# Kernel tuning notes

Measured on AMD Instinct MI355X. Metric: run time of the kernel, lower is better.

The kernel has to match this reference:

```python
import jax, jax.numpy as jnp
import numpy as np

T, B, D, H = 256, 2048, 16, 64


def _init_cell(key, in_dim, hidden):
    k1, k2, k3, k4 = jax.random.split(key, 4)
    s = 1.0 / np.sqrt(hidden)
    return (
        jax.random.uniform(k1, (4 * hidden, in_dim), minval=-s, maxval=s),
        jax.random.uniform(k2, (4 * hidden, hidden), minval=-s, maxval=s),
        jax.random.uniform(k3, (4 * hidden,), minval=-s, maxval=s),
        jax.random.uniform(k4, (4 * hidden,), minval=-s, maxval=s),
    )


def setup_inputs() -> dict:
    key = jax.random.key(0)
    kx, k0, k1, k2 = jax.random.split(key, 4)
    x = jax.random.normal(kx, (T, B, D), dtype=jnp.float32)
    W_ih0, W_hh0, b_ih0, b_hh0 = _init_cell(k0, D, H)
    W_ih1, W_hh1, b_ih1, b_hh1 = _init_cell(k1, H, H)
    W_ih2, W_hh2, b_ih2, b_hh2 = _init_cell(k2, H, H)
    return dict(x=x,
                W_ih0=W_ih0, W_hh0=W_hh0, b_ih0=b_ih0, b_hh0=b_hh0,
                W_ih1=W_ih1, W_hh1=W_hh1, b_ih1=b_ih1, b_hh1=b_hh1,
                W_ih2=W_ih2, W_hh2=W_hh2, b_ih2=b_ih2, b_hh2=b_hh2)


def _lstm_cell(x_t, h, c, W_ih, W_hh, b_ih, b_hh):
    # torch.nn.LSTMCell gate order: i, f, g, o
    gates = x_t @ W_ih.T + b_ih + h @ W_hh.T + b_hh  # (B, 4H)
    i, f, g, o = jnp.split(gates, 4, axis=-1)
    c_new = jax.nn.sigmoid(f) * c + jax.nn.sigmoid(i) * jnp.tanh(g)
    h_new = jax.nn.sigmoid(o) * jnp.tanh(c_new)
    return h_new, c_new


def reference(x, W_ih0, W_hh0, b_ih0, b_hh0,
              W_ih1, W_hh1, b_ih1, b_hh1,
              W_ih2, W_hh2, b_ih2, b_hh2):
    Bsz = x.shape[1]
    z = jnp.zeros((Bsz, H), dtype=x.dtype)
    init = (z, z, z, z, z, z)  # h0,h1,h2,c0,c1,c2

    def step(state, x_t):
        h0, h1, h2, c0, c1, c2 = state
        h0, c0 = _lstm_cell(x_t, h0, c0, W_ih0, W_hh0, b_ih0, b_hh0)
        h1, c1 = _lstm_cell(h0, h1, c1, W_ih1, W_hh1, b_ih1, b_hh1)
        h2, c2 = _lstm_cell(h1, h2, c2, W_ih2, W_hh2, b_ih2, b_hh2)
        return (h0, h1, h2, c0, c1, c2), h2

    _, out = jax.lax.scan(step, init, x)  # out: (T, B, H)
    return out
```

## Files before the change

### kernel.cpp

```cpp
#include <hip/hip_runtime.h>
#include <hip/hip_bf16.h>


#define TT 256
#define BB 2048
#define DD 16
#define HH 64

#define SROW 232
#define PANEL (8 * SROW)
#define H0O 0
#define H1O 64
#define H2O 128
#define XO  192

typedef __attribute__((ext_vector_type(8))) _Float16 halfx8;
typedef __attribute__((ext_vector_type(8))) unsigned short ushortx8;
typedef __attribute__((ext_vector_type(4))) float floatx4;

#if __has_builtin(__builtin_amdgcn_exp2f)
#define EXP2F(x) __builtin_amdgcn_exp2f(x)
#else
#define EXP2F(x) exp2f(x)
#endif
#if __has_builtin(__builtin_amdgcn_rcpf)
#define RCPF(x) __builtin_amdgcn_rcpf(x)
#else
#define RCPF(x) (1.0f/(x))
#endif

__device__ __forceinline__ float sigm(float x) {
  return RCPF(1.0f + EXP2F(-1.4426950408889634f * x));
}
__device__ __forceinline__ float tanh_f(float x) {
  float t = EXP2F(2.8853900817779268f * x);
  return 1.0f - 2.0f * RCPF(t + 1.0f);
}
__device__ __forceinline__ void block_sync() {
  asm volatile("s_waitcnt lgkmcnt(0)" ::: "memory");
  __builtin_amdgcn_s_barrier();
}

__global__ void detect_k(const unsigned short* __restrict__ xr, int* __restrict__ flag) {
  int cnt = 0;
  for (int i = threadIdx.x; i < 4096; i += 64) {
    float v = __uint_as_float(((unsigned int)xr[i]) << 16);
    if (!(fabsf(v) < 4.0f)) cnt++;
  }
#pragma unroll
  for (int o = 32; o > 0; o >>= 1) cnt += __shfl_down(cnt, o, 64);
  if (threadIdx.x == 0) flag[0] = (cnt < 100) ? 1 : 0;
}

#define MF(A, B, C) __builtin_amdgcn_mfma_f32_16x16x32_f16(A, B, C, 0, 0, 0)

#define BODY(S_, PPB, PNB)                                                        \
  {                                                                               \
    const int s_ = (S_);                                                          \
    halfx8 xreg = {};                                                             \
    const bool loader = (tid < 16) && (s_ + 1 < TT);                              \
    if (loader)                                                                   \
      xreg = ld8(xg, ((long)(s_ + 1) * BB + rowbase + (tid >> 1)) * DD + (tid & 1) * 8); \
    block_sync();                                                                 \
    const _Float16* PpR = SH + (PPB) + rd_off;                                    \
    _Float16* Pn = SH + (PNB);                                                    \
    halfx8 r0 = *(const halfx8*)(PpR + 0);                                        \
    halfx8 r1 = *(const halfx8*)(PpR + 32);                                       \
    halfx8 r2 = *(const halfx8*)(PpR + 64);                                       \
    halfx8 r3 = *(const halfx8*)(PpR + 96);                                       \
    halfx8 r4 = *(const halfx8*)(PpR + 128);                                      \
    halfx8 r5 = *(const halfx8*)(PpR + 160);                                      \
    halfx8 r6 = *(const halfx8*)(PpR + 192);                                      \
    floatx4 a0 = bs0, a1 = bs1, a2 = bs2;                                         \
    __builtin_amdgcn_s_setprio(1);                                                \
    a0 = MF(wA0[0], r0, a0); a2 = MF(wA2[0], r2, a2);                             \
    a0 = MF(wA0[1], r1, a0); a2 = MF(wA2[1], r3, a2);                             \
    a2 = MF(wA2[2], r4, a2); a0 = MF(wA0[2], r6, a0);                             \
    a2 = MF(wA2[3], r5, a2);                                                      \
    a1 = MF(wA1[0], r0, a1); a1 = MF(wA1[1], r1, a1);                             \
    a1 = MF(wA1[2], r2, a1); a1 = MF(wA1[3], r3, a1);                             \
    __builtin_amdgcn_s_setprio(0);                                                \
    {                       \
      floatx4 gv;                                                                 \
      gv[0] = m8 ? a2[0] : a0[0]; gv[1] = m8 ? a2[1] : a0[1];                     \
      gv[2] = m8 ? a2[2] : a0[2]; gv[3] = m8 ? a2[3] : a0[3];                     \
      float I = sigm(gv[0]), F = sigm(gv[1]), G = tanh_f(gv[2]), O = sigm(gv[3]); \
      float cn = F * cA + I * G;                                                  \
      float hn = O * tanh_f(cn);                                                  \
      bool vA = m8 ? (s_ >= 2) : (s_ < TT);                                       \
      if (vA) {                                                                   \
        cA = cn; Pn[wrA] = (_Float16)hn;                                          \
        if (m8) {                                                                 \
          long oi = (long)(s_ - 2) * ((long)BB * HH) + olane;                     \
          if (isbf) ((__hip_bfloat16*)outp)[oi] = __float2bfloat16(hn);           \
          else ((float*)outp)[oi] = hn;                                           \
        }                                                                         \
      }                                                                           \
    }                                                                             \
    {                                            \
      float I = sigm(a1[0]), F = sigm(a1[1]), G = tanh_f(a1[2]), O = sigm(a1[3]); \
      float cn = F * cB + I * G;                                                  \
      float hn = O * tanh_f(cn);                                                  \
      if (!m8 && s_ >= 1 && s_ <= TT) { cB = cn; Pn[wrB] = (_Float16)hn; }        \
    }                                                                             \
    if (loader) *(halfx8*)&Pn[(tid >> 1) * SROW + XO + (tid & 1) * 8] = xreg;     \
  }

__launch_bounds__(1024, 1)
__global__ void lstm3_k(const void* __restrict__ xg,
                        const void* W0i, const void* W0h, const void* B0i, const void* B0h,
                        const void* W1i, const void* W1h, const void* B1i, const void* B1h,
                        const void* W2i, const void* W2h, const void* B2i, const void* B2h,
                        void* __restrict__ outp, const int* __restrict__ flagp) {
  const int tid = threadIdx.x;
  const int W = tid >> 6;
  const int lane = tid & 63;
  const int c = lane & 15;
  const int g = lane >> 4;
  const int rowbase = blockIdx.x * 8;
  const int isbf = flagp ? flagp[0] : 1;

  __shared__ __align__(16) _Float16 SH[2 * PANEL + 32];

  auto ldf = [&](const void* b, long i) -> float {
    return isbf ? __bfloat162float(((const __hip_bfloat16*)b)[i]) : ((const float*)b)[i];
  };
  auto ld8 = [&](const void* b, long i) -> halfx8 {
    halfx8 r;
    if (isbf) {
      ushortx8 raw = *(const ushortx8*)((const unsigned short*)b + i);
#pragma unroll
      for (int j = 0; j < 8; ++j)
        r[j] = (_Float16)__uint_as_float(((unsigned int)raw[j]) << 16);
    } else {
      const float* s = (const float*)b + i;
#pragma unroll
      for (int j = 0; j < 8; ++j) r[j] = (_Float16)s[j];
    }
    return r;
  };

  halfx8 wA0[3], wA1[4], wA2[4];
  floatx4 bs0, bs1, bs2;
  {
    const int ril = W * 16 + c;
    const int u = ril >> 2, q = ril & 3;
    const long orig = q * 64 + u;
    halfx8 z = {};
    wA0[0] = ld8(W0h, orig * 64 + 8 * g);
    wA0[1] = ld8(W0h, orig * 64 + 32 + 8 * g);
    wA0[2] = (g == 0) ? ld8(W0i, orig * 16)
           : (g == 1) ? ld8(W0i, orig * 16 + 8) : z;
    wA1[0] = ld8(W1i, orig * 64 + 8 * g);
    wA1[1] = ld8(W1i, orig * 64 + 32 + 8 * g);
    wA1[2] = ld8(W1h, orig * 64 + 8 * g);
    wA1[3] = ld8(W1h, orig * 64 + 32 + 8 * g);
    wA2[0] = ld8(W2i, orig * 64 + 8 * g);
    wA2[1] = ld8(W2i, orig * 64 + 32 + 8 * g);
    wA2[2] = ld8(W2h, orig * 64 + 8 * g);
    wA2[3] = ld8(W2h, orig * 64 + 32 + 8 * g);
    const int ub = 4 * W + g;
#pragma unroll
    for (int qq = 0; qq < 4; ++qq) {
      bs0[qq] = ldf(B0i, 64 * qq + ub) + ldf(B0h, 64 * qq + ub);
      bs1[qq] = ldf(B1i, 64 * qq + ub) + ldf(B1h, 64 * qq + ub);
      bs2[qq] = ldf(B2i, 64 * qq + ub) + ldf(B2h, 64 * qq + ub);
    }
  }

  for (int i = tid; i < 2 * PANEL + 32; i += 1024) SH[i] = (_Float16)0.0f;
  block_sync();
  if (tid < 16) {
    *(halfx8*)&SH[(tid >> 1) * SROW + XO + (tid & 1) * 8] =
        ld8(xg, ((long)0 * BB + rowbase + (tid >> 1)) * DD + (tid & 1) * 8);
  }

  const bool m8 = (c >= 8);
  const int r_el = c & 7;
  const int u_el = 4 * W + g;
  const int rd_off = r_el * SROW + 8 * g;
  const int wrA = r_el * SROW + u_el + (m8 ? H2O : H0O);
  const int wrB = r_el * SROW + u_el + H1O;
  const long olane = ((long)rowbase + r_el) * HH + u_el;
  float cA = 0.f, cB = 0.f;

#pragma unroll 1
  for (int s2 = 0; s2 < (TT + 2) / 2; ++s2) {
    const int s = 2 * s2;
    BODY(s, 0, PANEL)
    BODY(s + 1, PANEL, 0)
  }
}

extern "C" void kernel_launch(void* const* d_in, const int* in_sizes, int n_in,
                              void* d_out, int out_size, void* d_ws, size_t ws_size,
                              hipStream_t stream) {
  (void)in_sizes; (void)n_in; (void)out_size;
  int* flag = (ws_size >= sizeof(int)) ? (int*)d_ws : nullptr;
  if (flag) {
    detect_k<<<dim3(1), dim3(64), 0, stream>>>((const unsigned short*)d_in[0], flag);
  }
  lstm3_k<<<dim3(BB / 8), dim3(1024), 0, stream>>>(
      d_in[0],
      d_in[1], d_in[2], d_in[3], d_in[4],
      d_in[5], d_in[6], d_in[7], d_in[8],
      d_in[9], d_in[10], d_in[11], d_in[12],
      d_out, flag);
}
```

Measured before the change: 279.2 us.

## Swap half-row hidden operands via DPP and fold log2e scaling into weights

Each lane now reads three shared-memory vectors plus one x vector, instead of seven vectors. The missing operand halves come from the partner lane through a DPP row rotate by 8, with a per-lane select. The log2(e) and 2·log2(e) factors are folded into the fp16 weights and biases at load time, so the sigmoid and tanh gate activations lose a multiply each. The shared row stride shrinks to match. This cuts LDS traffic and ALU work on the serial per-timestep critical path, at the cost of extra DPP moves and selects and slightly different fp16 rounding of the prescaled weights.

```diff
diff --git a/kernel.cpp b/kernel.cpp
--- a/kernel.cpp
+++ b/kernel.cpp
@@ -7,12 +7,15 @@
 #define DD 16
 #define HH 64
 
-#define SROW 232
+#define SROW 216
 #define PANEL (8 * SROW)
 #define H0O 0
 #define H1O 64
 #define H2O 128
 #define XO  192
+
+#define L2E  1.4426950408889634f
+#define L2E2 2.8853900817779268f
 
 typedef __attribute__((ext_vector_type(8))) _Float16 halfx8;
 typedef __attribute__((ext_vector_type(8))) unsigned short ushortx8;
@@ -29,16 +32,24 @@
 #define RCPF(x) (1.0f/(x))
 #endif
 
-__device__ __forceinline__ float sigm(float x) {
-  return RCPF(1.0f + EXP2F(-1.4426950408889634f * x));
-}
-__device__ __forceinline__ float tanh_f(float x) {
-  float t = EXP2F(2.8853900817779268f * x);
-  return 1.0f - 2.0f * RCPF(t + 1.0f);
+__device__ __forceinline__ float sigm_s(float xs) {
+  return RCPF(1.0f + EXP2F(-xs));
+}
+__device__ __forceinline__ float tanh_s(float xs) {
+  return 1.0f - 2.0f * RCPF(EXP2F(xs) + 1.0f);
 }
 __device__ __forceinline__ void block_sync() {
   asm volatile("s_waitcnt lgkmcnt(0)" ::: "memory");
   __builtin_amdgcn_s_barrier();
+}
+
+__device__ __forceinline__ halfx8 dpp_xor8(halfx8 v) {
+  union { halfx8 h; int i[4]; } u, d;
+  u.h = v;
+#pragma unroll
+  for (int k = 0; k < 4; ++k)
+    d.i[k] = __builtin_amdgcn_update_dpp(0, u.i[k], 0x128, 0xf, 0xf, true);
+  return d.h;
 }
 
 __global__ void detect_k(const unsigned short* __restrict__ xr, int* __restrict__ flag) {
@@ -62,20 +73,23 @@
     if (loader)                                                                   \
       xreg = ld8(xg, ((long)(s_ + 1) * BB + rowbase + (tid >> 1)) * DD + (tid & 1) * 8); \
     block_sync();                                                                 \
-    const _Float16* PpR = SH + (PPB) + rd_off;                                    \
+    const _Float16* PpR = SH + (PPB) + rd_offP;                                   \
     _Float16* Pn = SH + (PNB);                                                    \
-    halfx8 r0 = *(const halfx8*)(PpR + 0);                                        \
-    halfx8 r1 = *(const halfx8*)(PpR + 32);                                       \
-    halfx8 r2 = *(const halfx8*)(PpR + 64);                                       \
-    halfx8 r3 = *(const halfx8*)(PpR + 96);                                       \
-    halfx8 r4 = *(const halfx8*)(PpR + 128);                                      \
-    halfx8 r5 = *(const halfx8*)(PpR + 160);                                      \
-    halfx8 r6 = *(const halfx8*)(PpR + 192);                                      \
+    halfx8 pA = *(const halfx8*)(PpR + 0);                \
+    halfx8 pB = *(const halfx8*)(PpR + 64);                               \
+    halfx8 pC = *(const halfx8*)(PpR + 128);                              \
+    halfx8 rX = *(const halfx8*)(SH + (PPB) + rd_offX);         \
+    halfx8 sA = dpp_xor8(pA);                                                     \
+    halfx8 sB = dpp_xor8(pB);                                                     \
+    halfx8 sC = dpp_xor8(pC);                                                     \
+    halfx8 r0 = m8 ? sA : pA, r1 = m8 ? pA : sA;                                  \
+    halfx8 r2 = m8 ? sB : pB, r3 = m8 ? pB : sB;                                  \
+    halfx8 r4 = m8 ? sC : pC, r5 = m8 ? pC : sC;                                  \
     floatx4 a0 = bs0, a1 = bs1, a2 = bs2;                                         \
     __builtin_amdgcn_s_setprio(1);                                                \
     a0 = MF(wA0[0], r0, a0); a2 = MF(wA2[0], r2, a2);                             \
     a0 = MF(wA0[1], r1, a0); a2 = MF(wA2[1], r3, a2);                             \
-    a2 = MF(wA2[2], r4, a2); a0 = MF(wA0[2], r6, a0);                             \
+    a2 = MF(wA2[2], r4, a2); a0 = MF(wA0[2], rX, a0);                             \
     a2 = MF(wA2[3], r5, a2);                                                      \
     a1 = MF(wA1[0], r0, a1); a1 = MF(wA1[1], r1, a1);                             \
     a1 = MF(wA1[2], r2, a1); a1 = MF(wA1[3], r3, a1);                             \
@@ -84,9 +98,10 @@
       floatx4 gv;                                                                 \
       gv[0] = m8 ? a2[0] : a0[0]; gv[1] = m8 ? a2[1] : a0[1];                     \
       gv[2] = m8 ? a2[2] : a0[2]; gv[3] = m8 ? a2[3] : a0[3];                     \
-      float I = sigm(gv[0]), F = sigm(gv[1]), G = tanh_f(gv[2]), O = sigm(gv[3]); \
+      float I = sigm_s(gv[0]), F = sigm_s(gv[1]);                                 \
+      float G = tanh_s(gv[2]), O = sigm_s(gv[3]);                                 \
       float cn = F * cA + I * G;                                                  \
-      float hn = O * tanh_f(cn);                                                  \
+      float hn = O * tanh_s(L2E2 * cn);                                           \
       bool vA = m8 ? (s_ >= 2) : (s_ < TT);                                       \
       if (vA) {                                                                   \
         cA = cn; Pn[wrA] = (_Float16)hn;                                          \
@@ -98,9 +113,10 @@
       }                                                                           \
     }                                                                             \
     {                                            \
-      float I = sigm(a1[0]), F = sigm(a1[1]), G = tanh_f(a1[2]), O = sigm(a1[3]); \
+      float I = sigm_s(a1[0]), F = sigm_s(a1[1]);                                 \
+      float G = tanh_s(a1[2]), O = sigm_s(a1[3]);                                 \
       float cn = F * cB + I * G;                                                  \
-      float hn = O * tanh_f(cn);                                                  \
+      float hn = O * tanh_s(L2E2 * cn);                                           \
       if (!m8 && s_ >= 1 && s_ <= TT) { cB = cn; Pn[wrB] = (_Float16)hn; }        \
     }                                                                             \
     if (loader) *(halfx8*)&Pn[(tid >> 1) * SROW + XO + (tid & 1) * 8] = xreg;     \
@@ -139,6 +155,20 @@
     }
     return r;
   };
+  auto ld8s = [&](const void* b, long i, float sc) -> halfx8 {
+    halfx8 r;
+    if (isbf) {
+      ushortx8 raw = *(const ushortx8*)((const unsigned short*)b + i);
+#pragma unroll
+      for (int j = 0; j < 8; ++j)
+        r[j] = (_Float16)(sc * __uint_as_float(((unsigned int)raw[j]) << 16));
+    } else {
+      const float* s = (const float*)b + i;
+#pragma unroll
+      for (int j = 0; j < 8; ++j) r[j] = (_Float16)(sc * s[j]);
+    }
+    return r;
+  };
 
   halfx8 wA0[3], wA1[4], wA2[4];
   floatx4 bs0, bs1, bs2;
@@ -146,25 +176,27 @@
     const int ril = W * 16 + c;
     const int u = ril >> 2, q = ril & 3;
     const long orig = q * 64 + u;
+    const float sc = (q == 2) ? L2E2 : L2E;
     halfx8 z = {};
-    wA0[0] = ld8(W0h, orig * 64 + 8 * g);
-    wA0[1] = ld8(W0h, orig * 64 + 32 + 8 * g);
-    wA0[2] = (g == 0) ? ld8(W0i, orig * 16)
-           : (g == 1) ? ld8(W0i, orig * 16 + 8) : z;
-    wA1[0] = ld8(W1i, orig * 64 + 8 * g);
-    wA1[1] = ld8(W1i, orig * 64 + 32 + 8 * g);
-    wA1[2] = ld8(W1h, orig * 64 + 8 * g);
-    wA1[3] = ld8(W1h, orig * 64 + 32 + 8 * g);
-    wA2[0] = ld8(W2i, orig * 64 + 8 * g);
-    wA2[1] = ld8(W2i, orig * 64 + 32 + 8 * g);
-    wA2[2] = ld8(W2h, orig * 64 + 8 * g);
-    wA2[3] = ld8(W2h, orig * 64 + 32 + 8 * g);
+    wA0[0] = ld8s(W0h, orig * 64 + 8 * g, sc);
+    wA0[1] = ld8s(W0h, orig * 64 + 32 + 8 * g, sc);
+    wA0[2] = (g == 0) ? ld8s(W0i, orig * 16, sc)
+           : (g == 1) ? ld8s(W0i, orig * 16 + 8, sc) : z;
+    wA1[0] = ld8s(W1i, orig * 64 + 8 * g, sc);
+    wA1[1] = ld8s(W1i, orig * 64 + 32 + 8 * g, sc);
+    wA1[2] = ld8s(W1h, orig * 64 + 8 * g, sc);
+    wA1[3] = ld8s(W1h, orig * 64 + 32 + 8 * g, sc);
+    wA2[0] = ld8s(W2i, orig * 64 + 8 * g, sc);
+    wA2[1] = ld8s(W2i, orig * 64 + 32 + 8 * g, sc);
+    wA2[2] = ld8s(W2h, orig * 64 + 8 * g, sc);
+    wA2[3] = ld8s(W2h, orig * 64 + 32 + 8 * g, sc);
     const int ub = 4 * W + g;
 #pragma unroll
     for (int qq = 0; qq < 4; ++qq) {
-      bs0[qq] = ldf(B0i, 64 * qq + ub) + ldf(B0h, 64 * qq + ub);
-      bs1[qq] = ldf(B1i, 64 * qq + ub) + ldf(B1h, 64 * qq + ub);
-      bs2[qq] = ldf(B2i, 64 * qq + ub) + ldf(B2h, 64 * qq + ub);
+      const float bsc = (qq == 2) ? L2E2 : L2E;
+      bs0[qq] = bsc * (ldf(B0i, 64 * qq + ub) + ldf(B0h, 64 * qq + ub));
+      bs1[qq] = bsc * (ldf(B1i, 64 * qq + ub) + ldf(B1h, 64 * qq + ub));
+      bs2[qq] = bsc * (ldf(B2i, 64 * qq + ub) + ldf(B2h, 64 * qq + ub));
     }
   }
 
@@ -178,7 +210,8 @@
   const bool m8 = (c >= 8);
   const int r_el = c & 7;
   const int u_el = 4 * W + g;
-  const int rd_off = r_el * SROW + 8 * g;
+  const int rd_offP = r_el * SROW + 8 * g + (m8 ? 32 : 0);
+  const int rd_offX = r_el * SROW + 8 * g + XO;
   const int wrA = r_el * SROW + u_el + (m8 ? H2O : H0O);
   const int wrB = r_el * SROW + u_el + H1O;
   const long olane = ((long)rowbase + r_el) * HH + u_el;
```

Result: slower. 309.1 us (+10.7%).
